# Kernel optimization log

Hardware: AMD Instinct MI355X
Metric: run time of the kernel (lower is better)

Reference implementation:

```python
import jax, jax.numpy as jnp
import numpy as np

EPS = 1e-8


def setup_inputs() -> dict:
    key = jax.random.key(0)
    k1, k2, k3, k4 = jax.random.split(key, 4)
    batch, n_obs, hist = 64, 2048, 512
    values = jax.random.normal(k1, (batch, n_obs, hist), dtype=jnp.float32)
    means = jax.random.normal(k2, (n_obs,), dtype=jnp.float32)
    counts = jax.random.randint(k3, (n_obs,), 0, 1000, dtype=jnp.int32)
    # M2 = var * count, keep it positive and roughly scaled with count
    M2s = jax.random.uniform(k4, (n_obs,), dtype=jnp.float32) * counts.astype(jnp.float32)
    sig_ids = jnp.arange(n_obs, dtype=jnp.int32)  # one unique signature per obs column
    return {"values": values, "means": means, "M2s": M2s, "counts": counts, "sig_ids": sig_ids}


def reference(values, means, M2s, counts, sig_ids):
    """Training-mode forward: Welford merge of running per-signature stats with the
    batch of last-timestep values, then normalize full history with merged stats.

    values: [b, n, h] float; means/M2s: [n_sigs]; counts: [n_sigs] int; sig_ids: [n] int.
    """
    b = values.shape[0]
    v = values[:, :, -1]                      # [b, n] last timestep per obs
    mean_new = jnp.mean(v, axis=0)            # [n]
    var_new = jnp.var(v, axis=0)              # biased (ddof=0), matches unbiased=False
    count_new = jnp.float32(b)
    M2_new = var_new * count_new              # [n]

    # gather prior stats per observation column
    c = counts[sig_ids].astype(jnp.float32)   # [n]
    m = means[sig_ids]                        # [n]
    M2 = M2s[sig_ids]                         # [n]

    # Welford parallel merge (matches update())
    delta = mean_new - m
    total = c + count_new
    m_merged = m + delta * (count_new / total)
    M2_merged = M2 + M2_new + delta * delta * c * count_new / total

    # stats are stored detached (torch.no_grad + .detach())
    m_merged = jax.lax.stop_gradient(m_merged)
    M2_merged = jax.lax.stop_gradient(M2_merged)
    total = jax.lax.stop_gradient(total)

    var = M2_merged / total
    std = jnp.sqrt(var + EPS)                 # [n]
    normed = (values - m_merged[None, :, None]) / std[None, :, None]
    # count < 2 -> passthrough (matches normalize())
    ok = (total >= 2.0)[None, :, None]
    return jnp.where(ok, normed, values)
```

## Files before the change

### kernel.cpp

```cpp
#include <hip/hip_runtime.h>
#include <math.h>

#define EPS 1e-8f

__global__ void sig_stats_kernel(const float* __restrict__ values,
                                 const float* __restrict__ means,
                                 const float* __restrict__ M2s,
                                 const int* __restrict__ counts,
                                 const int* __restrict__ sig_ids,
                                 float* __restrict__ scale,
                                 float* __restrict__ shift,
                                 int n_obs, int hist, int batch) {
    int wave = (int)((blockIdx.x * blockDim.x + threadIdx.x) >> 6);
    int lane = (int)(threadIdx.x & 63);
    if (wave >= n_obs) return;

    float v = 0.0f;
    if (lane < batch) {
        long long idx = (long long)lane * n_obs * hist + (long long)wave * hist + (hist - 1);
        v = values[idx];
    }

    float s = v;
    #pragma unroll
    for (int o = 32; o > 0; o >>= 1) s += __shfl_xor(s, o, 64);
    float cnt_new = (float)batch;
    float mean_new = s / cnt_new;

    float d = (lane < batch) ? (v - mean_new) : 0.0f;
    float sq = d * d;
    #pragma unroll
    for (int o = 32; o > 0; o >>= 1) sq += __shfl_xor(sq, o, 64);
    float M2_new = sq;

    if (lane == 0) {
        int id = sig_ids[wave];
        float c  = (float)counts[id];
        float m  = means[id];
        float M2 = M2s[id];
        float delta = mean_new - m;
        float total = c + cnt_new;
        float m_merged  = m + delta * (cnt_new / total);
        float M2_merged = M2 + M2_new + delta * delta * c * cnt_new / total;
        float var = M2_merged / total;
        float stdv = sqrtf(var + EPS);
        bool ok = (total >= 2.0f);
        float sc = ok ? (1.0f / stdv) : 1.0f;
        float sh = ok ? (-m_merged / stdv) : 0.0f;
        scale[wave] = sc;
        shift[wave] = sh;
    }
}

__global__ void sig_norm_kernel(const float4* __restrict__ vals,
                                const float* __restrict__ scale,
                                const float* __restrict__ shift,
                                float4* __restrict__ out,
                                int n_obs, int h4) {
    int row = blockIdx.x;
    int n = row % n_obs;
    float s = scale[n];
    float t = shift[n];
    long long base = (long long)row * h4;
    for (int j = threadIdx.x; j < h4; j += blockDim.x) {
        float4 v = vals[base + j];
        float4 o;
        o.x = fmaf(v.x, s, t);
        o.y = fmaf(v.y, s, t);
        o.z = fmaf(v.z, s, t);
        o.w = fmaf(v.w, s, t);
        out[base + j] = o;
    }
}

extern "C" void kernel_launch(void* const* d_in, const int* in_sizes, int n_in,
                              void* d_out, int out_size, void* d_ws, size_t ws_size,
                              hipStream_t stream) {
    const float* values  = (const float*)d_in[0];
    const float* means   = (const float*)d_in[1];
    const float* M2s     = (const float*)d_in[2];
    const int*   counts  = (const int*)d_in[3];
    const int*   sig_ids = (const int*)d_in[4];
    float* out = (float*)d_out;

    const int batch = 64;
    int n_obs = in_sizes[1];
    long long total = (long long)in_sizes[0];
    int hist = (int)(total / ((long long)batch * n_obs));

    float* scale = (float*)d_ws;
    float* shift = scale + n_obs;

    int waves_per_block = 4;
    int blocks1 = (n_obs + waves_per_block - 1) / waves_per_block;
    sig_stats_kernel<<<blocks1, 256, 0, stream>>>(values, means, M2s, counts, sig_ids,
                                                  scale, shift, n_obs, hist, batch);

    int h4 = hist / 4;
    int rows = batch * n_obs;
    sig_norm_kernel<<<rows, 128, 0, stream>>>((const float4*)values, scale, shift,
                                              (float4*)out, n_obs, h4);
}
```

Before: 430.4 us.

## Use persistent grid-stride waves per row and pack scale/shift into float2

Result: slower. 444.5 us (+3.3%).

```diff
diff --git a/kernel.cpp b/kernel.cpp
--- a/kernel.cpp
+++ b/kernel.cpp
@@ -8,8 +8,7 @@
                                  const float* __restrict__ M2s,
                                  const int* __restrict__ counts,
                                  const int* __restrict__ sig_ids,
-                                 float* __restrict__ scale,
-                                 float* __restrict__ shift,
+                                 float2* __restrict__ ss,
                                  int n_obs, int hist, int batch) {
     int wave = (int)((blockIdx.x * blockDim.x + threadIdx.x) >> 6);
     int lane = (int)(threadIdx.x & 63);
@@ -47,29 +46,32 @@
         bool ok = (total >= 2.0f);
         float sc = ok ? (1.0f / stdv) : 1.0f;
         float sh = ok ? (-m_merged / stdv) : 0.0f;
-        scale[wave] = sc;
-        shift[wave] = sh;
+        ss[wave] = make_float2(sc, sh);
     }
 }
 
-__global__ void sig_norm_kernel(const float4* __restrict__ vals,
-                                const float* __restrict__ scale,
-                                const float* __restrict__ shift,
-                                float4* __restrict__ out,
-                                int n_obs, int h4) {
-    int row = blockIdx.x;
-    int n = row % n_obs;
-    float s = scale[n];
-    float t = shift[n];
-    long long base = (long long)row * h4;
-    for (int j = threadIdx.x; j < h4; j += blockDim.x) {
-        float4 v = vals[base + j];
-        float4 o;
-        o.x = fmaf(v.x, s, t);
-        o.y = fmaf(v.y, s, t);
-        o.z = fmaf(v.z, s, t);
-        o.w = fmaf(v.w, s, t);
-        out[base + j] = o;
+__global__ __launch_bounds__(256) void sig_norm_kernel(const float4* __restrict__ vals,
+                                                       const float2* __restrict__ ss,
+                                                       float4* __restrict__ out,
+                                                       int n_obs, int h4, int rows) {
+    int gwave  = (int)((blockIdx.x * blockDim.x + threadIdx.x) >> 6);
+    int lane   = (int)(threadIdx.x & 63);
+    int nwaves = (int)((gridDim.x * blockDim.x) >> 6);
+
+    for (int row = gwave; row < rows; row += nwaves) {
+        int n = row % n_obs;
+        float2 st = ss[n];
+        long long base = (long long)row * h4;
+        #pragma unroll 2
+        for (int j = lane; j < h4; j += 64) {
+            float4 v = vals[base + j];
+            float4 o;
+            o.x = fmaf(v.x, st.x, st.y);
+            o.y = fmaf(v.y, st.x, st.y);
+            o.z = fmaf(v.z, st.x, st.y);
+            o.w = fmaf(v.w, st.x, st.y);
+            out[base + j] = o;
+        }
     }
 }
 
@@ -88,16 +90,16 @@
     long long total = (long long)in_sizes[0];
     int hist = (int)(total / ((long long)batch * n_obs));
 
-    float* scale = (float*)d_ws;
-    float* shift = scale + n_obs;
+    float2* ss = (float2*)d_ws;
 
     int waves_per_block = 4;
     int blocks1 = (n_obs + waves_per_block - 1) / waves_per_block;
     sig_stats_kernel<<<blocks1, 256, 0, stream>>>(values, means, M2s, counts, sig_ids,
-                                                  scale, shift, n_obs, hist, batch);
+                                                  ss, n_obs, hist, batch);
 
     int h4 = hist / 4;
     int rows = batch * n_obs;
-    sig_norm_kernel<<<rows, 128, 0, stream>>>((const float4*)values, scale, shift,
-                                              (float4*)out, n_obs, h4);
+    int blocks2 = 2048;
+    sig_norm_kernel<<<blocks2, 256, 0, stream>>>((const float4*)values, ss,
+                                                 (float4*)out, n_obs, h4, rows);
 }
```
